# Kernel tuning notes

Measured on AMD Instinct MI355X. Metric: run time of the kernel, lower is better.

Reference implementation:

```python
import jax, jax.numpy as jnp
import numpy as np

K = 32
D = 64
N_ITER = 10


def setup_inputs() -> dict:
    key = jax.random.key(0)
    k1, k2 = jax.random.split(key)
    B = 65536
    x = jax.random.normal(k1, (B, D), dtype=jnp.float32)
    c = jnp.zeros((K,), dtype=jnp.float32)
    mu = jax.random.normal(k2, (K, D), dtype=jnp.float32) * 0.1
    A = jnp.tile(jnp.eye(D, dtype=jnp.float32)[None], (K, 1, 1))
    alpha = jnp.float32(0.1)
    return {"x": x, "c": c, "mu": mu, "A": A, "alpha": alpha}


def _grad_phi(x, c, mu, A):
    # Precision matrices Sigma_i^{-1} = A_i^T A_i : (k, d, d)
    P = jnp.einsum('kji,kjl->kil', A, A)
    diff = x[:, None, :] - mu[None, :, :]          # (B, k, d)
    Pd = jnp.einsum('kij,bkj->bki', P, diff)       # Sigma^{-1} (x - mu)
    quad = jnp.einsum('bki,bki->bk', diff, Pd)     # (B, k)
    # Analytic gradient of phi(x) = logsumexp_i(c_i - 0.5 q_i):
    # grad = -sum_i softmax_i(c_i - 0.5 q_i) * Sigma_i^{-1}(x - mu_i)
    w = jax.nn.softmax(c[None, :] - 0.5 * quad, axis=1)  # (B, k)
    return -jnp.einsum('bk,bki->bi', w, Pd)


def reference(x, c, mu, A, alpha):
    def step(x_cur, _):
        x_new = x_cur + alpha * _grad_phi(x_cur, c, mu, A)
        return x_new, None
    x_final, _ = jax.lax.scan(step, x, None, length=N_ITER)
    return x_final
```

## Files before the change

kernel.cpp:

```cpp
#include <hip/hip_runtime.h>
#include <hip/hip_bf16.h>


typedef __attribute__((ext_vector_type(4))) float f32x4;
typedef __attribute__((ext_vector_type(8))) short bf16x8;

#define KC 32
#define NITER 10
#define XROW 72
#define WT_PITCH 40
#define PW_BYTES 7168

static __device__ __forceinline__ unsigned pk_bf16(float a, float b) {
  __hip_bfloat16 ha = __float2bfloat16(a), hb = __float2bfloat16(b);
  unsigned short ua = *(unsigned short*)&ha, ub = *(unsigned short*)&hb;
  return (unsigned)ua | ((unsigned)ub << 16);
}

static __device__ __forceinline__ float red16(float x) {
  int v = __builtin_amdgcn_ds_swizzle(__float_as_int(x), 0x401F);
  return x + __int_as_float(v);
}
static __device__ __forceinline__ float red32(float x) {
  int xi = __float_as_int(x);
  auto pr = __builtin_amdgcn_permlane32_swap(xi, xi, false, false);
  return __int_as_float(pr[0]) + __int_as_float(pr[1]);
}

__global__ void precompute1(const float* __restrict__ A, const float* __restrict__ mu,
                            const float* __restrict__ c,
                            float* __restrict__ Pmu_g, float* __restrict__ e_g,
                            __hip_bfloat16* __restrict__ Psw) {
  __shared__ float As[64 * 64];
  __shared__ float Pk[64 * 64];
  const int k = blockIdx.x, tid = threadIdx.x;
  const float* Ak = A + k * 4096;
  for (int idx = tid; idx < 1024; idx += 256)
    *(f32x4*)&As[idx * 4] = *(const f32x4*)&Ak[idx * 4];
  __syncthreads();

  const int i = tid >> 2, lg = tid & 3;
  float acc[16] = {};
  for (int j = 0; j < 64; ++j) {
    float ai = As[j * 64 + i];
    const f32x4* row = (const f32x4*)&As[j * 64 + lg * 16];
#pragma unroll
    for (int g = 0; g < 4; ++g) {
      f32x4 v = row[g];
#pragma unroll
      for (int r = 0; r < 4; ++r) acc[g * 4 + r] += ai * v[r];
    }
  }
#pragma unroll
  for (int g = 0; g < 4; ++g)
#pragma unroll
    for (int r = 0; r < 4; ++r) Pk[i * 64 + lg * 16 + g * 4 + r] = acc[g * 4 + r];
  __syncthreads();

  if (tid < 64) {
    float s = 0.f;
    for (int l = 0; l < 64; ++l) s += Pk[l * 64 + tid] * mu[k * 64 + l];
    Pmu_g[k * 64 + tid] = s;
    float v = mu[k * 64 + tid] * s;
#pragma unroll
    for (int off = 1; off < 64; off <<= 1) v += __shfl_xor(v, off, 64);
    if (tid == 0) e_g[k] = c[k] - 0.5f * v;
  }

  unsigned* Psw32 = (unsigned*)(Psw + k * 4096);
  for (int idx2 = tid; idx2 < 2048; idx2 += 256) {
    int idx = idx2 << 1;
    int f = idx >> 9, ln = (idx >> 3) & 63, j = idx & 7;
    int mt = f >> 1, s = f & 1, qq = ln >> 4, l4 = ln & 15;
    int col = mt * 16 + l4, rb = s * 32 + qq * 8 + j;
    Psw32[idx2] = pk_bf16(Pk[rb * 64 + col], Pk[(rb + 1) * 64 + col]);
  }
}

__global__ void precompute2(const float* __restrict__ Pmu_g,
                            __hip_bfloat16* __restrict__ PmuA,
                            __hip_bfloat16* __restrict__ PmuB) {
  const int tid = threadIdx.x;
  for (int idx = tid; idx < 2048; idx += 256) {
    int f = idx >> 9, lane = (idx >> 3) & 63, j = idx & 7;
    int mtc = f >> 1, s = f & 1, qq = lane >> 4, l4 = lane & 15;
    PmuA[idx] = __float2bfloat16(Pmu_g[(mtc * 16 + l4) * 64 + s * 32 + qq * 8 + j]);
  }
  for (int idx = tid; idx < 2048; idx += 256) {
    int f = idx >> 9, lane = (idx >> 3) & 63, j = idx & 7;
    int qq = lane >> 4, l4 = lane & 15;
    PmuB[idx] = __float2bfloat16(Pmu_g[(qq * 8 + j) * 64 + f * 16 + l4]);
  }
}

__launch_bounds__(256, 2)
__global__ void denoise_main(const float* __restrict__ x_in,
                             const float* __restrict__ e_g,
                             const float* __restrict__ alpha_g,
                             const __hip_bfloat16* __restrict__ Psw,
                             const __hip_bfloat16* __restrict__ PmuA,
                             const __hip_bfloat16* __restrict__ PmuB,
                             float* __restrict__ out) {
  __shared__ __attribute__((aligned(16))) char scratch[4 * PW_BYTES];

  const int tid = threadIdx.x;
  const int wave = tid >> 6, lane = tid & 63;
  const int q = lane >> 4, l4 = lane & 15;
  const int base_pt = blockIdx.x * 128 + wave * 32;
  const float alpha = alpha_g[0];

  char* pw = scratch + wave * PW_BYTES;
  __hip_bfloat16* xsw = (__hip_bfloat16*)pw;
  float* pmxw = (float*)pw;
  __hip_bfloat16* wtw = (__hip_bfloat16*)(pw + 4608);

  const bf16x8* PswF = (const bf16x8*)Psw;
  const bf16x8* PmuAF = (const bf16x8*)PmuA;
  const bf16x8* PmuBF = (const bf16x8*)PmuB;

  f32x4 xm[4][2];
#pragma unroll
  for (int mt = 0; mt < 4; ++mt)
#pragma unroll
    for (int nt = 0; nt < 2; ++nt)
      xm[mt][nt] = *(const f32x4*)&x_in[(base_pt + nt * 16 + l4) * 64 + mt * 16 + q * 4];

  f32x4 ev[2];
#pragma unroll
  for (int mtc = 0; mtc < 2; ++mtc) ev[mtc] = *(const f32x4*)&e_g[mtc * 16 + q * 4];

  const f32x4 Z4 = {0.f, 0.f, 0.f, 0.f};

#pragma unroll 1
  for (int it = 0; it < NITER; ++it) {
#pragma unroll
    for (int mt = 0; mt < 4; ++mt)
#pragma unroll
      for (int nt = 0; nt < 2; ++nt) {
        uint2 v;
        v.x = pk_bf16(xm[mt][nt][0], xm[mt][nt][1]);
        v.y = pk_bf16(xm[mt][nt][2], xm[mt][nt][3]);
        *(uint2*)&xsw[(nt * 16 + l4) * XROW + mt * 16 + q * 4] = v;
      }

    bf16x8 bx[2][2];
#pragma unroll
    for (int s = 0; s < 2; ++s)
#pragma unroll
      for (int nt = 0; nt < 2; ++nt)
        bx[s][nt] = *(const bf16x8*)&xsw[(nt * 16 + l4) * XROW + s * 32 + q * 8];

    bf16x8 ap[2][4][2];
#pragma unroll
    for (int mt = 0; mt < 4; ++mt)
#pragma unroll
      for (int s = 0; s < 2; ++s)
        ap[0][mt][s] = PswF[(mt * 2 + s) * 64 + lane];

    f32x4 pmx[2][2];
#pragma unroll
    for (int mtc = 0; mtc < 2; ++mtc)
#pragma unroll
      for (int nt = 0; nt < 2; ++nt) {
        f32x4 acc = Z4;
#pragma unroll
        for (int s = 0; s < 2; ++s) {
          bf16x8 a = PmuAF[(mtc * 2 + s) * 64 + lane];
          acc = __builtin_amdgcn_mfma_f32_16x16x32_bf16(a, bx[s][nt], acc, 0, 0, 0);
        }
        pmx[mtc][nt] = acc;
      }
#pragma unroll
    for (int mtc = 0; mtc < 2; ++mtc)
#pragma unroll
      for (int nt = 0; nt < 2; ++nt)
#pragma unroll
        for (int r = 0; r < 4; ++r)
          pmxw[(mtc * 16 + q * 4 + r) * 32 + nt * 16 + l4] = pmx[mtc][nt][r] + ev[mtc][r];

    f32x4 accY[4][2];
#pragma unroll
    for (int mt = 0; mt < 4; ++mt)
#pragma unroll
      for (int nt = 0; nt < 2; ++nt) accY[mt][nt] = Z4;
    float lsum0 = 0.f, lsum1 = 0.f;

#pragma unroll 2
    for (int k = 0; k < KC; ++k) {
      const int cur = k & 1, nxt = cur ^ 1;
      const int kn = (k + 1) & (KC - 1);
#pragma unroll
      for (int mt = 0; mt < 4; ++mt)
#pragma unroll
        for (int s = 0; s < 2; ++s)
          ap[nxt][mt][s] = PswF[kn * 512 + (mt * 2 + s) * 64 + lane];

      f32x4 y[4][2];
#pragma unroll
      for (int mt = 0; mt < 4; ++mt)
#pragma unroll
        for (int nt = 0; nt < 2; ++nt) {
          f32x4 acc = Z4;
          acc = __builtin_amdgcn_mfma_f32_16x16x32_bf16(ap[cur][mt][0], bx[0][nt], acc, 0, 0, 0);
          acc = __builtin_amdgcn_mfma_f32_16x16x32_bf16(ap[cur][mt][1], bx[1][nt], acc, 0, 0, 0);
          y[mt][nt] = acc;
        }

      f32x4 d0 = xm[0][0] * y[0][0];
      f32x4 d1 = xm[0][1] * y[0][1];
#pragma unroll
      for (int mt = 1; mt < 4; ++mt) {
        d0 += xm[mt][0] * y[mt][0];
        d1 += xm[mt][1] * y[mt][1];
      }
      float xy0 = (d0[0] + d0[1]) + (d0[2] + d0[3]);
      float xy1 = (d1[0] + d1[1]) + (d1[2] + d1[3]);
      xy0 = red32(red16(xy0));
      xy1 = red32(red16(xy1));

      const float pk0 = pmxw[k * 32 + l4];
      const float pk1 = pmxw[k * 32 + 16 + l4];
      const float w0 = __expf(pk0 - 0.5f * xy0);
      const float w1 = __expf(pk1 - 0.5f * xy1);
      lsum0 += w0;
      lsum1 += w1;
      if (q == 0) {
        wtw[l4 * WT_PITCH + k] = __float2bfloat16(w0);
        wtw[(16 + l4) * WT_PITCH + k] = __float2bfloat16(w1);
      }
#pragma unroll
      for (int mt = 0; mt < 4; ++mt) {
        accY[mt][0] += w0 * y[mt][0];
        accY[mt][1] += w1 * y[mt][1];
      }
    }

    bf16x8 wtf[2];
#pragma unroll
    for (int nt = 0; nt < 2; ++nt)
      wtf[nt] = *(const bf16x8*)&wtw[(nt * 16 + l4) * WT_PITCH + q * 8];
    f32x4 pacc[4][2];
#pragma unroll
    for (int mt = 0; mt < 4; ++mt) {
      bf16x8 a = PmuBF[mt * 64 + lane];
      pacc[mt][0] = __builtin_amdgcn_mfma_f32_16x16x32_bf16(a, wtf[0], Z4, 0, 0, 0);
      pacc[mt][1] = __builtin_amdgcn_mfma_f32_16x16x32_bf16(a, wtf[1], Z4, 0, 0, 0);
    }

    const float c0 = alpha / lsum0;
    const float c1 = alpha / lsum1;
#pragma unroll
    for (int mt = 0; mt < 4; ++mt) {
      xm[mt][0] += c0 * (pacc[mt][0] - accY[mt][0]);
      xm[mt][1] += c1 * (pacc[mt][1] - accY[mt][1]);
    }
  }

#pragma unroll
  for (int mt = 0; mt < 4; ++mt)
#pragma unroll
    for (int nt = 0; nt < 2; ++nt)
      *(f32x4*)&out[(base_pt + nt * 16 + l4) * 64 + mt * 16 + q * 4] = xm[mt][nt];
}

extern "C" void kernel_launch(void* const* d_in, const int* in_sizes, int n_in,
                              void* d_out, int out_size, void* d_ws, size_t ws_size,
                              hipStream_t stream) {
  (void)in_sizes; (void)n_in; (void)out_size; (void)ws_size;
  const float* x = (const float*)d_in[0];
  const float* c = (const float*)d_in[1];
  const float* mu = (const float*)d_in[2];
  const float* A = (const float*)d_in[3];
  const float* alpha = (const float*)d_in[4];
  float* out = (float*)d_out;

  char* ws = (char*)d_ws;
  float* Pmu_g = (float*)(ws);
  float* e_g = (float*)(ws + 8192);
  __hip_bfloat16* PmuA = (__hip_bfloat16*)(ws + 8448);
  __hip_bfloat16* PmuB = (__hip_bfloat16*)(ws + 12544);
  __hip_bfloat16* Psw = (__hip_bfloat16*)(ws + 16640);

  precompute1<<<32, 256, 0, stream>>>(A, mu, c, Pmu_g, e_g, Psw);
  precompute2<<<1, 256, 0, stream>>>(Pmu_g, PmuA, PmuB);
  denoise_main<<<512, 256, 0, stream>>>(x, e_g, alpha, Psw, PmuA, PmuB, out);
}
```

Baseline: 290.5 us.

## Stage per-component precision tiles into shared LDS via global_load_lds double buffer

The 8 KB bf16 precision tile for component k+1 is now loaded cooperatively by all four waves into a double-buffered LDS region with global_load_lds, instead of each wave fetching its own copy from global memory into registers. Every wave then reads its MFMA A-operands from LDS, and a block barrier after each component keeps the buffers in order. This aims to cut redundant global/L1 traffic and register pressure from the old register double buffer. The cost is 32 extra barriers per outer iteration and more LDS per block. The xy reduction also changes: red16 uses permlane16_swap when available, and the two partial dot-product sums are computed as a 2-wide vector.

New measurement: 307.6 us. 1.06x slower.

```diff
diff --git a/kernel.cpp b/kernel.cpp
--- a/kernel.cpp
+++ b/kernel.cpp
@@ -2,6 +2,7 @@
 #include <hip/hip_bf16.h>
 
 
+typedef __attribute__((ext_vector_type(2))) float f32x2;
 typedef __attribute__((ext_vector_type(4))) float f32x4;
 typedef __attribute__((ext_vector_type(8))) short bf16x8;
 
@@ -10,6 +11,7 @@
 #define XROW 72
 #define WT_PITCH 40
 #define PW_BYTES 7168
+#define PSTG 8192
 
 static __device__ __forceinline__ unsigned pk_bf16(float a, float b) {
   __hip_bfloat16 ha = __float2bfloat16(a), hb = __float2bfloat16(b);
@@ -18,13 +20,25 @@
 }
 
 static __device__ __forceinline__ float red16(float x) {
+#if __has_builtin(__builtin_amdgcn_permlane16_swap)
+  int xi = __float_as_int(x);
+  auto pr = __builtin_amdgcn_permlane16_swap(xi, xi, false, false);
+  return __int_as_float(pr[0]) + __int_as_float(pr[1]);
+#else
   int v = __builtin_amdgcn_ds_swizzle(__float_as_int(x), 0x401F);
   return x + __int_as_float(v);
+#endif
 }
 static __device__ __forceinline__ float red32(float x) {
   int xi = __float_as_int(x);
   auto pr = __builtin_amdgcn_permlane32_swap(xi, xi, false, false);
   return __int_as_float(pr[0]) + __int_as_float(pr[1]);
+}
+
+static __device__ __forceinline__ void stage16(const void* gsrc, void* ldst) {
+  __builtin_amdgcn_global_load_lds(
+      (const __attribute__((address_space(1))) unsigned int*)gsrc,
+      (__attribute__((address_space(3))) unsigned int*)ldst, 16, 0, 0);
 }
 
 __global__ void precompute1(const float* __restrict__ A, const float* __restrict__ mu,
@@ -101,7 +115,7 @@
                              const __hip_bfloat16* __restrict__ PmuA,
                              const __hip_bfloat16* __restrict__ PmuB,
                              float* __restrict__ out) {
-  __shared__ __attribute__((aligned(16))) char scratch[4 * PW_BYTES];
+  __shared__ __attribute__((aligned(16))) char scratch[4 * PW_BYTES + 2 * PSTG];
 
   const int tid = threadIdx.x;
   const int wave = tid >> 6, lane = tid & 63;
@@ -113,8 +127,9 @@
   __hip_bfloat16* xsw = (__hip_bfloat16*)pw;
   float* pmxw = (float*)pw;
   __hip_bfloat16* wtw = (__hip_bfloat16*)(pw + 4608);
-
-  const bf16x8* PswF = (const bf16x8*)Psw;
+  char* pstg = scratch + 4 * PW_BYTES;
+
+  const char* PswB = (const char*)Psw;
   const bf16x8* PmuAF = (const bf16x8*)PmuA;
   const bf16x8* PmuBF = (const bf16x8*)PmuB;
 
@@ -130,9 +145,13 @@
   for (int mtc = 0; mtc < 2; ++mtc) ev[mtc] = *(const f32x4*)&e_g[mtc * 16 + q * 4];
 
   const f32x4 Z4 = {0.f, 0.f, 0.f, 0.f};
+  const int f0 = 2 * wave, f1 = 2 * wave + 1;
 
 #pragma unroll 1
   for (int it = 0; it < NITER; ++it) {
+    stage16(PswB + f0 * 1024 + lane * 16, pstg + f0 * 1024);
+    stage16(PswB + f1 * 1024 + lane * 16, pstg + f1 * 1024);
+
 #pragma unroll
     for (int mt = 0; mt < 4; ++mt)
 #pragma unroll
@@ -150,13 +169,6 @@
       for (int nt = 0; nt < 2; ++nt)
         bx[s][nt] = *(const bf16x8*)&xsw[(nt * 16 + l4) * XROW + s * 32 + q * 8];
 
-    bf16x8 ap[2][4][2];
-#pragma unroll
-    for (int mt = 0; mt < 4; ++mt)
-#pragma unroll
-      for (int s = 0; s < 2; ++s)
-        ap[0][mt][s] = PswF[(mt * 2 + s) * 64 + lane];
-
     f32x4 pmx[2][2];
 #pragma unroll
     for (int mtc = 0; mtc < 2; ++mtc)
@@ -185,15 +197,25 @@
       for (int nt = 0; nt < 2; ++nt) accY[mt][nt] = Z4;
     float lsum0 = 0.f, lsum1 = 0.f;
 
+    __syncthreads();
+
 #pragma unroll 2
     for (int k = 0; k < KC; ++k) {
-      const int cur = k & 1, nxt = cur ^ 1;
-      const int kn = (k + 1) & (KC - 1);
+      const int cur = k & 1;
+      if (k < KC - 1) {
+        const char* ps = PswB + (k + 1) * PSTG;
+        char* pd = pstg + (cur ^ 1) * PSTG;
+        stage16(ps + f0 * 1024 + lane * 16, pd + f0 * 1024);
+        stage16(ps + f1 * 1024 + lane * 16, pd + f1 * 1024);
+      }
+
+      const char* pc = pstg + cur * PSTG;
+      bf16x8 ap[4][2];
 #pragma unroll
       for (int mt = 0; mt < 4; ++mt)
 #pragma unroll
         for (int s = 0; s < 2; ++s)
-          ap[nxt][mt][s] = PswF[kn * 512 + (mt * 2 + s) * 64 + lane];
+          ap[mt][s] = *(const bf16x8*)(pc + (mt * 2 + s) * 1024 + lane * 16);
 
       f32x4 y[4][2];
 #pragma unroll
@@ -201,8 +223,8 @@
 #pragma unroll
         for (int nt = 0; nt < 2; ++nt) {
           f32x4 acc = Z4;
-          acc = __builtin_amdgcn_mfma_f32_16x16x32_bf16(ap[cur][mt][0], bx[0][nt], acc, 0, 0, 0);
-          acc = __builtin_amdgcn_mfma_f32_16x16x32_bf16(ap[cur][mt][1], bx[1][nt], acc, 0, 0, 0);
+          acc = __builtin_amdgcn_mfma_f32_16x16x32_bf16(ap[mt][0], bx[0][nt], acc, 0, 0, 0);
+          acc = __builtin_amdgcn_mfma_f32_16x16x32_bf16(ap[mt][1], bx[1][nt], acc, 0, 0, 0);
           y[mt][nt] = acc;
         }
 
@@ -213,10 +235,10 @@
         d0 += xm[mt][0] * y[mt][0];
         d1 += xm[mt][1] * y[mt][1];
       }
-      float xy0 = (d0[0] + d0[1]) + (d0[2] + d0[3]);
-      float xy1 = (d1[0] + d1[1]) + (d1[2] + d1[3]);
-      xy0 = red32(red16(xy0));
-      xy1 = red32(red16(xy1));
+      f32x2 h = __builtin_shufflevector(d0, d1, 0, 4) + __builtin_shufflevector(d0, d1, 1, 5) +
+                __builtin_shufflevector(d0, d1, 2, 6) + __builtin_shufflevector(d0, d1, 3, 7);
+      const float xy0 = red32(red16(h[0]));
+      const float xy1 = red32(red16(h[1]));
 
       const float pk0 = pmxw[k * 32 + l4];
       const float pk1 = pmxw[k * 32 + 16 + l4];
@@ -233,6 +255,8 @@
         accY[mt][0] += w0 * y[mt][0];
         accY[mt][1] += w1 * y[mt][1];
       }
+
+      __syncthreads();
     }
 
     bf16x8 wtf[2];
```
